# Optimization experiments

Hardware: AMD Instinct MI355X
Metric: run time of the kernel (lower is better)

Reference implementation:

```python
import jax, jax.numpy as jnp
import numpy as np

N_NODES = 50000
N_EDGES = 1600000
IN_FEAT = 256
HIDDEN = 128
N_CLASSES = 16


def gcn_conv(x, edge_index, W, b, n_nodes):
    """PyG GCNConv: x' = D^{-1/2} (A+I) D^{-1/2} (x @ W) + b."""
    h = x @ W  # project first (PyG order), messages are in out_dim
    src, dst = edge_index[0], edge_index[1]
    loops = jnp.arange(n_nodes, dtype=src.dtype)
    src = jnp.concatenate([src, loops])
    dst = jnp.concatenate([dst, loops])
    # degree of A+I (count incoming edges incl. self loop)
    deg = jax.ops.segment_sum(jnp.ones_like(dst, dtype=h.dtype), dst, num_segments=n_nodes)
    dis = jax.lax.rsqrt(deg)  # deg >= 1 thanks to self loops
    norm = dis[src] * dis[dst]  # [E+N]
    msgs = h[src] * norm[:, None]  # gather + scale
    out = jax.ops.segment_sum(msgs, dst, num_segments=n_nodes)  # scatter-add
    return out + b


def setup_inputs() -> dict:
    key = jax.random.key(0)
    k_x, k_e, k_w1, k_b1, k_w2, k_b2 = jax.random.split(key, 6)
    x = jax.random.normal(k_x, (N_NODES, IN_FEAT), dtype=jnp.float32)
    edge_index = jax.random.randint(k_e, (2, N_EDGES), 0, N_NODES, dtype=jnp.int64)
    s1 = 1.0 / np.sqrt(IN_FEAT)
    s2 = 1.0 / np.sqrt(HIDDEN)
    W1 = jax.random.uniform(k_w1, (IN_FEAT, HIDDEN), jnp.float32, -s1, s1)
    b1 = jax.random.uniform(k_b1, (HIDDEN,), jnp.float32, -s1, s1)
    W2 = jax.random.uniform(k_w2, (HIDDEN, N_CLASSES), jnp.float32, -s2, s2)
    b2 = jax.random.uniform(k_b2, (N_CLASSES,), jnp.float32, -s2, s2)
    return {"x": x, "edge_index": edge_index, "W1": W1, "b1": b1, "W2": W2, "b2": b2}


def reference(x, edge_index, W1, b1, W2, b2):
    n = x.shape[0]
    h = gcn_conv(x, edge_index, W1, b1, n)
    h = jax.nn.relu(h)
    logits = gcn_conv(h, edge_index, W2, b2, n)
    return logits, jax.nn.softmax(logits, axis=1)
```

## Files before the change

kernel.cpp:

```cpp
#include <hip/hip_runtime.h>
#include <hip/hip_bf16.h>
#include <math.h>

#define N_NODES 50000
#define N_EDGES 1600000
#define IN_FEAT 256
#define HIDDEN 128
#define N_CLASSES 16

#define ECHUNK 8192
#define NCHK 196
#define NBKT 196

typedef __attribute__((ext_vector_type(8))) short short8;
typedef __attribute__((ext_vector_type(4))) float floatx4;

__device__ __forceinline__ unsigned short f2bf(float f) {
    unsigned u = __float_as_uint(f);
    return (unsigned short)((u + 0x7fffu + ((u >> 16) & 1u)) >> 16);
}

__device__ __forceinline__ unsigned pk2bf(float a, float b) {
    __hip_bfloat162 h = __float22bfloat162_rn(make_float2(a, b));
    union { __hip_bfloat162 h; unsigned u; } cv;
    cv.h = h;
    return cv.u;
}


__global__ __launch_bounds__(256) void edge_hist(const int* __restrict__ dst,
                                                 int* __restrict__ hist,
                                                 const float* __restrict__ W1,
                                                 unsigned short* __restrict__ w1t) {
    __shared__ int h[256];
    int t = threadIdx.x;
    h[t] = 0;
    if (blockIdx.x < HIDDEN)
        w1t[blockIdx.x * IN_FEAT + t] = f2bf(W1[t * HIDDEN + blockIdx.x]);
    __syncthreads();
    int base = blockIdx.x * ECHUNK;
    int end = min(base + ECHUNK, N_EDGES);
    for (int i = base + t; i < end; i += 256)
        atomicAdd(&h[dst[i] >> 8], 1);
    __syncthreads();
    hist[blockIdx.x * 256 + t] = h[t];
}

__global__ __launch_bounds__(256) void scan_hist(int* __restrict__ hist,
                                                 int* __restrict__ bucket_base) {
    __shared__ int tot[256];
    int b = threadIdx.x;
    int sum = 0;
    for (int c = 0; c < NCHK; ++c) sum += hist[c * 256 + b];
    int v = sum;
    tot[b] = sum;
    __syncthreads();
    for (int off = 1; off < 256; off <<= 1) {
        int x = (b >= off) ? tot[b - off] : 0;
        __syncthreads();
        tot[b] += x;
        __syncthreads();
    }
    int excl = tot[b] - v;
    bucket_base[b] = excl;
    int run = excl;
    for (int c = 0; c < NCHK; ++c) {
        int h = hist[c * 256 + b];
        hist[c * 256 + b] = run;
        run += h;
    }
}

__global__ __launch_bounds__(256) void scatter_edges(const int* __restrict__ src,
                                                     const int* __restrict__ dst,
                                                     const int* __restrict__ hist,
                                                     unsigned int* __restrict__ sorted) {
    __shared__ int cur[256];
    int t = threadIdx.x;
    cur[t] = hist[blockIdx.x * 256 + t];
    __syncthreads();
    int base = blockIdx.x * ECHUNK;
    int end = min(base + ECHUNK, N_EDGES);
    for (int i = base + t; i < end; i += 256) {
        int d = dst[i];
        int s = src[i];
        int pos = atomicAdd(&cur[d >> 8], 1);
        sorted[pos] = ((unsigned)d << 16) | (unsigned)s;
    }
}

__global__ __launch_bounds__(256) void build_csr(const unsigned int* __restrict__ sorted,
                                                 const int* __restrict__ bucket_base,
                                                 int* __restrict__ row_start,
                                                 float* __restrict__ dis,
                                                 unsigned short* __restrict__ csr_src) {
    __shared__ int cnt[256];
    __shared__ int roff[256];
    int t = threadIdx.x;
    int bkt = blockIdx.x;
    int ebase = bucket_base[bkt];
    int eend = (bkt == NBKT - 1) ? N_EDGES : bucket_base[bkt + 1];
    cnt[t] = 0;
    __syncthreads();
    for (int i = ebase + t; i < eend; i += 256)
        atomicAdd(&cnt[(sorted[i] >> 16) & 255], 1);
    __syncthreads();
    int v = cnt[t];
    roff[t] = v;
    __syncthreads();
    for (int off = 1; off < 256; off <<= 1) {
        int x = (t >= off) ? roff[t - off] : 0;
        __syncthreads();
        roff[t] += x;
        __syncthreads();
    }
    int excl = roff[t] - v;
    int node = bkt * 256 + t;
    if (node < N_NODES) {
        row_start[node] = ebase + excl;
        dis[node] = 1.0f / sqrtf((float)(v + 1));
        if (node == N_NODES - 1) row_start[N_NODES] = N_EDGES;
    }
    __syncthreads();
    cnt[t] = ebase + excl;
    __syncthreads();
    for (int i = ebase + t; i < eend; i += 256) {
        unsigned e = sorted[i];
        int pos = atomicAdd(&cnt[(e >> 16) & 255], 1);
        csr_src[pos] = (unsigned short)(e & 0xffffu);
    }
}

__global__ __launch_bounds__(256) void gemm1_mfma(const float* __restrict__ x,
                                                  const unsigned short* __restrict__ w1t,
                                                  const float* __restrict__ dis,
                                                  unsigned int* __restrict__ g1) {
    int tid = threadIdx.x;
    int w = tid >> 6;
    int lane = tid & 63;
    int quad = lane >> 4;
    int c = lane & 15;
    int row_base = blockIdx.x * 64 + (w >> 1) * 32;
    int col_base = (w & 1) * 64;

    floatx4 acc[2][4] = {};

    const float* xp[2];
#pragma unroll
    for (int rt = 0; rt < 2; ++rt) {
        int r = min(row_base + rt * 16 + c, N_NODES - 1);
        xp[rt] = x + (size_t)r * IN_FEAT + quad * 8;
    }
    const unsigned short* bp[4];
#pragma unroll
    for (int nt = 0; nt < 4; ++nt)
        bp[nt] = w1t + (size_t)(col_base + nt * 16 + c) * IN_FEAT + quad * 8;

#pragma unroll
    for (int k0 = 0; k0 < IN_FEAT; k0 += 32) {
        short8 a[2], b[4];
#pragma unroll
        for (int rt = 0; rt < 2; ++rt) {
            float4 f0 = *(const float4*)(xp[rt] + k0);
            float4 f1 = *(const float4*)(xp[rt] + k0 + 4);
            union { short8 s; unsigned u[4]; } au;
            au.u[0] = pk2bf(f0.x, f0.y);
            au.u[1] = pk2bf(f0.z, f0.w);
            au.u[2] = pk2bf(f1.x, f1.y);
            au.u[3] = pk2bf(f1.z, f1.w);
            a[rt] = au.s;
        }
#pragma unroll
        for (int nt = 0; nt < 4; ++nt)
            b[nt] = *(const short8*)(bp[nt] + k0);
#pragma unroll
        for (int rt = 0; rt < 2; ++rt)
#pragma unroll
            for (int nt = 0; nt < 4; ++nt)
                acc[rt][nt] = __builtin_amdgcn_mfma_f32_16x16x32_bf16(a[rt], b[nt], acc[rt][nt], 0, 0, 0);
    }

    bool evenlane = (lane & 1) == 0;
#pragma unroll
    for (int rt = 0; rt < 2; ++rt) {
#pragma unroll
        for (int reg = 0; reg < 4; ++reg) {
            int row = row_base + rt * 16 + quad * 4 + reg;
            float dv = dis[min(row, N_NODES - 1)];
#pragma unroll
            for (int nt = 0; nt < 4; ++nt) {
                float v = acc[rt][nt][reg] * dv;
                float vo = __shfl_xor(v, 1);
                if (evenlane && row < N_NODES) {
                    unsigned pkd = (unsigned)f2bf(v) | ((unsigned)f2bf(vo) << 16);
                    g1[(size_t)row * 64 + (col_base >> 1) + nt * 8 + (c >> 1)] = pkd;
                }
            }
        }
    }
}

__global__ __launch_bounds__(256) void agg1_gemm2(const unsigned int* __restrict__ g1,
                                                  const int* __restrict__ row_start,
                                                  const unsigned short* __restrict__ csr_src,
                                                  const float* __restrict__ dis,
                                                  const float* __restrict__ b1,
                                                  const float* __restrict__ W2,
                                                  float* __restrict__ g2) {
    __shared__ float w2s[HIDDEN * N_CLASSES];
    __shared__ float rs[4][HIDDEN];
    int tid = threadIdx.x;
    for (int i = tid; i < HIDDEN * N_CLASSES; i += 256) w2s[i] = W2[i];
    __syncthreads();

    int wave = tid >> 6;
    int lane = tid & 63;
    int node = blockIdx.x * 4 + wave;

    unsigned su = g1[(size_t)node * 64 + lane];
    float a0x = __uint_as_float(su << 16), a0y = __uint_as_float(su & 0xffff0000u);
    float a1x = 0.f, a1y = 0.f, a2x = 0.f, a2y = 0.f, a3x = 0.f, a3y = 0.f;
    float a4x = 0.f, a4y = 0.f, a5x = 0.f, a5y = 0.f, a6x = 0.f, a6y = 0.f, a7x = 0.f, a7y = 0.f;

    int e0 = row_start[node], e1 = row_start[node + 1];
    int e = e0;
    for (; e + 8 <= e1; e += 8) {
        int s0 = csr_src[e + 0], s1 = csr_src[e + 1], s2 = csr_src[e + 2], s3 = csr_src[e + 3];
        int s4 = csr_src[e + 4], s5 = csr_src[e + 5], s6 = csr_src[e + 6], s7 = csr_src[e + 7];
        unsigned u0 = g1[(size_t)s0 * 64 + lane];
        unsigned u1 = g1[(size_t)s1 * 64 + lane];
        unsigned u2 = g1[(size_t)s2 * 64 + lane];
        unsigned u3 = g1[(size_t)s3 * 64 + lane];
        unsigned u4 = g1[(size_t)s4 * 64 + lane];
        unsigned u5 = g1[(size_t)s5 * 64 + lane];
        unsigned u6 = g1[(size_t)s6 * 64 + lane];
        unsigned u7 = g1[(size_t)s7 * 64 + lane];
        a0x += __uint_as_float(u0 << 16); a0y += __uint_as_float(u0 & 0xffff0000u);
        a1x += __uint_as_float(u1 << 16); a1y += __uint_as_float(u1 & 0xffff0000u);
        a2x += __uint_as_float(u2 << 16); a2y += __uint_as_float(u2 & 0xffff0000u);
        a3x += __uint_as_float(u3 << 16); a3y += __uint_as_float(u3 & 0xffff0000u);
        a4x += __uint_as_float(u4 << 16); a4y += __uint_as_float(u4 & 0xffff0000u);
        a5x += __uint_as_float(u5 << 16); a5y += __uint_as_float(u5 & 0xffff0000u);
        a6x += __uint_as_float(u6 << 16); a6y += __uint_as_float(u6 & 0xffff0000u);
        a7x += __uint_as_float(u7 << 16); a7y += __uint_as_float(u7 & 0xffff0000u);
    }
    for (; e < e1; ++e) {
        int s = csr_src[e];
        unsigned u = g1[(size_t)s * 64 + lane];
        a0x += __uint_as_float(u << 16); a0y += __uint_as_float(u & 0xffff0000u);
    }
    float sx = ((a0x + a1x) + (a2x + a3x)) + ((a4x + a5x) + (a6x + a7x));
    float sy = ((a0y + a1y) + (a2y + a3y)) + ((a4y + a5y) + (a6y + a7y));

    float dv = dis[node];
    float2 bb = ((const float2*)b1)[lane];
    float rx = fmaxf(fmaf(dv, sx, bb.x), 0.f);
    float ry = fmaxf(fmaf(dv, sy, bb.y), 0.f);

    *(float2*)&rs[wave][lane * 2] = make_float2(rx, ry);

    int grp = lane >> 4;
    int c = lane & 15;
    int f0 = grp * 32;
    float p = 0.f;
#pragma unroll
    for (int k = 0; k < 32; ++k)
        p = fmaf(rs[wave][f0 + k], w2s[(f0 + k) * N_CLASSES + c], p);
    p += __shfl_xor(p, 16);
    p += __shfl_xor(p, 32);
    if (lane < 16) g2[(size_t)node * N_CLASSES + lane] = dv * p;
}

__global__ __launch_bounds__(256) void agg2_softmax(const float* __restrict__ g2,
                                                    const int* __restrict__ row_start,
                                                    const unsigned short* __restrict__ csr_src,
                                                    const float* __restrict__ dis,
                                                    const float* __restrict__ b2,
                                                    float* __restrict__ out) {
    int tid = threadIdx.x;
    int node = blockIdx.x * 16 + (tid >> 4);
    int c = tid & 15;
    float acc0 = g2[(size_t)node * N_CLASSES + c];
    float acc1 = 0.f, acc2 = 0.f, acc3 = 0.f;
    float acc4 = 0.f, acc5 = 0.f, acc6 = 0.f, acc7 = 0.f;
    int e0 = row_start[node], e1 = row_start[node + 1];
    int e = e0;
    for (; e + 8 <= e1; e += 8) {
        int s0 = csr_src[e + 0], s1 = csr_src[e + 1], s2 = csr_src[e + 2], s3 = csr_src[e + 3];
        int s4 = csr_src[e + 4], s5 = csr_src[e + 5], s6 = csr_src[e + 6], s7 = csr_src[e + 7];
        acc0 += g2[(size_t)s0 * N_CLASSES + c];
        acc1 += g2[(size_t)s1 * N_CLASSES + c];
        acc2 += g2[(size_t)s2 * N_CLASSES + c];
        acc3 += g2[(size_t)s3 * N_CLASSES + c];
        acc4 += g2[(size_t)s4 * N_CLASSES + c];
        acc5 += g2[(size_t)s5 * N_CLASSES + c];
        acc6 += g2[(size_t)s6 * N_CLASSES + c];
        acc7 += g2[(size_t)s7 * N_CLASSES + c];
    }
    for (; e < e1; ++e) {
        int s = csr_src[e];
        acc0 += g2[(size_t)s * N_CLASSES + c];
    }
    acc0 = ((acc0 + acc1) + (acc2 + acc3)) + ((acc4 + acc5) + (acc6 + acc7));
    float logit = fmaf(dis[node], acc0, b2[c]);
    out[(size_t)node * N_CLASSES + c] = logit;
    float m = logit;
    for (int off = 8; off; off >>= 1) m = fmaxf(m, __shfl_xor(m, off));
    float ex = expf(logit - m);
    float s = ex;
    for (int off = 8; off; off >>= 1) s += __shfl_xor(s, off);
    out[(size_t)N_NODES * N_CLASSES + (size_t)node * N_CLASSES + c] = ex / s;
}


extern "C" void kernel_launch(void* const* d_in, const int* in_sizes, int n_in,
                              void* d_out, int out_size, void* d_ws, size_t ws_size,
                              hipStream_t stream) {
    const float* x  = (const float*)d_in[0];
    const int*   ei = (const int*)d_in[1];
    const float* W1 = (const float*)d_in[2];
    const float* b1 = (const float*)d_in[3];
    const float* W2 = (const float*)d_in[4];
    const float* b2 = (const float*)d_in[5];
    float* out = (float*)d_out;

    char* ws = (char*)d_ws;
    size_t off = 0;
    auto alloc = [&](size_t bytes) -> char* {
        char* p = ws + off;
        off = (off + bytes + 511) & ~(size_t)511;
        return p;
    };
    int*   hist        = (int*)alloc((size_t)NCHK * 256 * 4);
    int*   bucket_base = (int*)alloc(256 * 4);
    float* dis         = (float*)alloc(N_NODES * 4);
    int*   row_start   = (int*)alloc((N_NODES + 1) * 4);
    unsigned short* w1t = (unsigned short*)alloc((size_t)HIDDEN * IN_FEAT * 2);
    unsigned short* csr_src = (unsigned short*)alloc((size_t)N_EDGES * 2);
    unsigned int* g1   = (unsigned int*)alloc((size_t)N_NODES * 64 * 4);
    float* g2          = (float*)alloc((size_t)N_NODES * N_CLASSES * 4);
    unsigned int* sorted = (unsigned int*)g1;
    (void)ws_size; (void)in_sizes; (void)n_in; (void)out_size;

    const int* src = ei;
    const int* dst = ei + N_EDGES;

    edge_hist<<<NCHK, 256, 0, stream>>>(dst, hist, W1, w1t);
    scan_hist<<<1, 256, 0, stream>>>(hist, bucket_base);
    scatter_edges<<<NCHK, 256, 0, stream>>>(src, dst, hist, sorted);
    build_csr<<<NBKT, 256, 0, stream>>>(sorted, bucket_base, row_start, dis, csr_src);

    gemm1_mfma<<<(N_NODES + 63) / 64, 256, 0, stream>>>(x, w1t, dis, g1);
    agg1_gemm2<<<N_NODES / 4, 256, 0, stream>>>(g1, row_start, csr_src, dis, b1, W2, g2);
    agg2_softmax<<<N_NODES / 16, 256, 0, stream>>>(g2, row_start, csr_src, dis, b2, out);
}
```

Before: 259.6 us.

## Replace histogram-scan edge sort with fixed-capacity atomic buckets; prefetch gemm1 operands

```diff
diff --git a/kernel.cpp b/kernel.cpp
--- a/kernel.cpp
+++ b/kernel.cpp
@@ -11,6 +11,7 @@
 #define ECHUNK 8192
 #define NCHK 196
 #define NBKT 196
+#define BCAP 10240
 
 typedef __attribute__((ext_vector_type(8))) short short8;
 typedef __attribute__((ext_vector_type(4))) float floatx4;
@@ -27,79 +28,48 @@
     return cv.u;
 }
 
-
-__global__ __launch_bounds__(256) void edge_hist(const int* __restrict__ dst,
-                                                 int* __restrict__ hist,
-                                                 const float* __restrict__ W1,
-                                                 unsigned short* __restrict__ w1t) {
-    __shared__ int h[256];
+__global__ __launch_bounds__(256) void scatter_edges2(const int* __restrict__ src,
+                                                      const int* __restrict__ dst,
+                                                      int* __restrict__ cursor,
+                                                      unsigned int* __restrict__ sorted,
+                                                      const float* __restrict__ W1,
+                                                      unsigned short* __restrict__ w1t) {
+    __shared__ int hloc[256];
     int t = threadIdx.x;
-    h[t] = 0;
+    hloc[t] = 0;
     if (blockIdx.x < HIDDEN)
         w1t[blockIdx.x * IN_FEAT + t] = f2bf(W1[t * HIDDEN + blockIdx.x]);
     __syncthreads();
     int base = blockIdx.x * ECHUNK;
     int end = min(base + ECHUNK, N_EDGES);
     for (int i = base + t; i < end; i += 256)
-        atomicAdd(&h[dst[i] >> 8], 1);
-    __syncthreads();
-    hist[blockIdx.x * 256 + t] = h[t];
-}
-
-__global__ __launch_bounds__(256) void scan_hist(int* __restrict__ hist,
-                                                 int* __restrict__ bucket_base) {
-    __shared__ int tot[256];
-    int b = threadIdx.x;
-    int sum = 0;
-    for (int c = 0; c < NCHK; ++c) sum += hist[c * 256 + b];
-    int v = sum;
-    tot[b] = sum;
-    __syncthreads();
-    for (int off = 1; off < 256; off <<= 1) {
-        int x = (b >= off) ? tot[b - off] : 0;
-        __syncthreads();
-        tot[b] += x;
-        __syncthreads();
-    }
-    int excl = tot[b] - v;
-    bucket_base[b] = excl;
-    int run = excl;
-    for (int c = 0; c < NCHK; ++c) {
-        int h = hist[c * 256 + b];
-        hist[c * 256 + b] = run;
-        run += h;
-    }
-}
-
-__global__ __launch_bounds__(256) void scatter_edges(const int* __restrict__ src,
-                                                     const int* __restrict__ dst,
-                                                     const int* __restrict__ hist,
-                                                     unsigned int* __restrict__ sorted) {
-    __shared__ int cur[256];
-    int t = threadIdx.x;
-    cur[t] = hist[blockIdx.x * 256 + t];
-    __syncthreads();
-    int base = blockIdx.x * ECHUNK;
-    int end = min(base + ECHUNK, N_EDGES);
+        atomicAdd(&hloc[dst[i] >> 8], 1);
+    __syncthreads();
+    int cnt = hloc[t];
+    int lbase = t * BCAP + atomicAdd(&cursor[t], cnt);
+    __syncthreads();
+    hloc[t] = lbase;
+    __syncthreads();
     for (int i = base + t; i < end; i += 256) {
         int d = dst[i];
         int s = src[i];
-        int pos = atomicAdd(&cur[d >> 8], 1);
+        int pos = atomicAdd(&hloc[d >> 8], 1);
         sorted[pos] = ((unsigned)d << 16) | (unsigned)s;
     }
 }
 
-__global__ __launch_bounds__(256) void build_csr(const unsigned int* __restrict__ sorted,
-                                                 const int* __restrict__ bucket_base,
-                                                 int* __restrict__ row_start,
-                                                 float* __restrict__ dis,
-                                                 unsigned short* __restrict__ csr_src) {
+__global__ __launch_bounds__(256) void build_csr2(const unsigned int* __restrict__ sorted,
+                                                  const int* __restrict__ cursor,
+                                                  int* __restrict__ rs,
+                                                  int* __restrict__ re,
+                                                  float* __restrict__ dis,
+                                                  unsigned short* __restrict__ csr_src) {
     __shared__ int cnt[256];
     __shared__ int roff[256];
     int t = threadIdx.x;
     int bkt = blockIdx.x;
-    int ebase = bucket_base[bkt];
-    int eend = (bkt == NBKT - 1) ? N_EDGES : bucket_base[bkt + 1];
+    int ebase = bkt * BCAP;
+    int eend = ebase + cursor[bkt];
     cnt[t] = 0;
     __syncthreads();
     for (int i = ebase + t; i < eend; i += 256)
@@ -117,9 +87,9 @@
     int excl = roff[t] - v;
     int node = bkt * 256 + t;
     if (node < N_NODES) {
-        row_start[node] = ebase + excl;
+        rs[node] = ebase + excl;
+        re[node] = ebase + excl + v;
         dis[node] = 1.0f / sqrtf((float)(v + 1));
-        if (node == N_NODES - 1) row_start[N_NODES] = N_EDGES;
     }
     __syncthreads();
     cnt[t] = ebase + excl;
@@ -156,28 +126,53 @@
     for (int nt = 0; nt < 4; ++nt)
         bp[nt] = w1t + (size_t)(col_base + nt * 16 + c) * IN_FEAT + quad * 8;
 
-#pragma unroll
-    for (int k0 = 0; k0 < IN_FEAT; k0 += 32) {
-        short8 a[2], b[4];
+    float4 fa[2][2];
+    short8 bcur[4];
+#pragma unroll
+    for (int rt = 0; rt < 2; ++rt) {
+        fa[rt][0] = *(const float4*)(xp[rt] + 0);
+        fa[rt][1] = *(const float4*)(xp[rt] + 4);
+    }
+#pragma unroll
+    for (int nt = 0; nt < 4; ++nt)
+        bcur[nt] = *(const short8*)(bp[nt] + 0);
+
+#pragma unroll
+    for (int kk = 0; kk < 8; ++kk) {
+        float4 fn[2][2];
+        short8 bn[4];
+        if (kk < 7) {
+            int k0n = (kk + 1) * 32;
+#pragma unroll
+            for (int rt = 0; rt < 2; ++rt) {
+                fn[rt][0] = *(const float4*)(xp[rt] + k0n);
+                fn[rt][1] = *(const float4*)(xp[rt] + k0n + 4);
+            }
+#pragma unroll
+            for (int nt = 0; nt < 4; ++nt)
+                bn[nt] = *(const short8*)(bp[nt] + k0n);
+        }
+        short8 a[2];
 #pragma unroll
         for (int rt = 0; rt < 2; ++rt) {
-            float4 f0 = *(const float4*)(xp[rt] + k0);
-            float4 f1 = *(const float4*)(xp[rt] + k0 + 4);
             union { short8 s; unsigned u[4]; } au;
-            au.u[0] = pk2bf(f0.x, f0.y);
-            au.u[1] = pk2bf(f0.z, f0.w);
-            au.u[2] = pk2bf(f1.x, f1.y);
-            au.u[3] = pk2bf(f1.z, f1.w);
+            au.u[0] = pk2bf(fa[rt][0].x, fa[rt][0].y);
+            au.u[1] = pk2bf(fa[rt][0].z, fa[rt][0].w);
+            au.u[2] = pk2bf(fa[rt][1].x, fa[rt][1].y);
+            au.u[3] = pk2bf(fa[rt][1].z, fa[rt][1].w);
             a[rt] = au.s;
         }
 #pragma unroll
-        for (int nt = 0; nt < 4; ++nt)
-            b[nt] = *(const short8*)(bp[nt] + k0);
-#pragma unroll
         for (int rt = 0; rt < 2; ++rt)
 #pragma unroll
             for (int nt = 0; nt < 4; ++nt)
-                acc[rt][nt] = __builtin_amdgcn_mfma_f32_16x16x32_bf16(a[rt], b[nt], acc[rt][nt], 0, 0, 0);
+                acc[rt][nt] = __builtin_amdgcn_mfma_f32_16x16x32_bf16(a[rt], bcur[nt], acc[rt][nt], 0, 0, 0);
+        if (kk < 7) {
+#pragma unroll
+            for (int rt = 0; rt < 2; ++rt) { fa[rt][0] = fn[rt][0]; fa[rt][1] = fn[rt][1]; }
+#pragma unroll
+            for (int nt = 0; nt < 4; ++nt) bcur[nt] = bn[nt];
+        }
     }
 
     bool evenlane = (lane & 1) == 0;
@@ -201,14 +196,15 @@
 }
 
 __global__ __launch_bounds__(256) void agg1_gemm2(const unsigned int* __restrict__ g1,
-                                                  const int* __restrict__ row_start,
+                                                  const int* __restrict__ rs,
+                                                  const int* __restrict__ re,
                                                   const unsigned short* __restrict__ csr_src,
                                                   const float* __restrict__ dis,
                                                   const float* __restrict__ b1,
                                                   const float* __restrict__ W2,
                                                   float* __restrict__ g2) {
     __shared__ float w2s[HIDDEN * N_CLASSES];
-    __shared__ float rs[4][HIDDEN];
+    __shared__ float rsh[4][HIDDEN];
     int tid = threadIdx.x;
     for (int i = tid; i < HIDDEN * N_CLASSES; i += 256) w2s[i] = W2[i];
     __syncthreads();
@@ -222,7 +218,7 @@
     float a1x = 0.f, a1y = 0.f, a2x = 0.f, a2y = 0.f, a3x = 0.f, a3y = 0.f;
     float a4x = 0.f, a4y = 0.f, a5x = 0.f, a5y = 0.f, a6x = 0.f, a6y = 0.f, a7x = 0.f, a7y = 0.f;
 
-    int e0 = row_start[node], e1 = row_start[node + 1];
+    int e0 = rs[node], e1 = re[node];
     int e = e0;
     for (; e + 8 <= e1; e += 8) {
         int s0 = csr_src[e + 0], s1 = csr_src[e + 1], s2 = csr_src[e + 2], s3 = csr_src[e + 3];
@@ -257,7 +253,7 @@
     float rx = fmaxf(fmaf(dv, sx, bb.x), 0.f);
     float ry = fmaxf(fmaf(dv, sy, bb.y), 0.f);
 
-    *(float2*)&rs[wave][lane * 2] = make_float2(rx, ry);
+    *(float2*)&rsh[wave][lane * 2] = make_float2(rx, ry);
 
     int grp = lane >> 4;
     int c = lane & 15;
@@ -265,14 +261,15 @@
     float p = 0.f;
 #pragma unroll
     for (int k = 0; k < 32; ++k)
-        p = fmaf(rs[wave][f0 + k], w2s[(f0 + k) * N_CLASSES + c], p);
+        p = fmaf(rsh[wave][f0 + k], w2s[(f0 + k) * N_CLASSES + c], p);
     p += __shfl_xor(p, 16);
     p += __shfl_xor(p, 32);
     if (lane < 16) g2[(size_t)node * N_CLASSES + lane] = dv * p;
 }
 
 __global__ __launch_bounds__(256) void agg2_softmax(const float* __restrict__ g2,
-                                                    const int* __restrict__ row_start,
+                                                    const int* __restrict__ rs,
+                                                    const int* __restrict__ re,
                                                     const unsigned short* __restrict__ csr_src,
                                                     const float* __restrict__ dis,
                                                     const float* __restrict__ b2,
@@ -283,7 +280,7 @@
     float acc0 = g2[(size_t)node * N_CLASSES + c];
     float acc1 = 0.f, acc2 = 0.f, acc3 = 0.f;
     float acc4 = 0.f, acc5 = 0.f, acc6 = 0.f, acc7 = 0.f;
-    int e0 = row_start[node], e1 = row_start[node + 1];
+    int e0 = rs[node], e1 = re[node];
     int e = e0;
     for (; e + 8 <= e1; e += 8) {
         int s0 = csr_src[e + 0], s1 = csr_src[e + 1], s2 = csr_src[e + 2], s3 = csr_src[e + 3];
@@ -331,26 +328,25 @@
         off = (off + bytes + 511) & ~(size_t)511;
         return p;
     };
-    int*   hist        = (int*)alloc((size_t)NCHK * 256 * 4);
-    int*   bucket_base = (int*)alloc(256 * 4);
-    float* dis         = (float*)alloc(N_NODES * 4);
-    int*   row_start   = (int*)alloc((N_NODES + 1) * 4);
+    int*   cursor   = (int*)alloc(256 * 4);
+    float* dis      = (float*)alloc(N_NODES * 4);
+    int*   rs       = (int*)alloc(N_NODES * 4);
+    int*   re       = (int*)alloc(N_NODES * 4);
     unsigned short* w1t = (unsigned short*)alloc((size_t)HIDDEN * IN_FEAT * 2);
-    unsigned short* csr_src = (unsigned short*)alloc((size_t)N_EDGES * 2);
-    unsigned int* g1   = (unsigned int*)alloc((size_t)N_NODES * 64 * 4);
-    float* g2          = (float*)alloc((size_t)N_NODES * N_CLASSES * 4);
+    unsigned short* csr_src = (unsigned short*)alloc((size_t)NBKT * BCAP * 2);
+    unsigned int* g1 = (unsigned int*)alloc((size_t)N_NODES * 64 * 4);
+    float* g2       = (float*)alloc((size_t)N_NODES * N_CLASSES * 4);
     unsigned int* sorted = (unsigned int*)g1;
     (void)ws_size; (void)in_sizes; (void)n_in; (void)out_size;
 
     const int* src = ei;
     const int* dst = ei + N_EDGES;
 
-    edge_hist<<<NCHK, 256, 0, stream>>>(dst, hist, W1, w1t);
-    scan_hist<<<1, 256, 0, stream>>>(hist, bucket_base);
-    scatter_edges<<<NCHK, 256, 0, stream>>>(src, dst, hist, sorted);
-    build_csr<<<NBKT, 256, 0, stream>>>(sorted, bucket_base, row_start, dis, csr_src);
+    hipMemsetAsync(cursor, 0, 256 * 4, stream);
+    scatter_edges2<<<NCHK, 256, 0, stream>>>(src, dst, cursor, sorted, W1, w1t);
+    build_csr2<<<NBKT, 256, 0, stream>>>(sorted, cursor, rs, re, dis, csr_src);
 
     gemm1_mfma<<<(N_NODES + 63) / 64, 256, 0, stream>>>(x, w1t, dis, g1);
-    agg1_gemm2<<<N_NODES / 4, 256, 0, stream>>>(g1, row_start, csr_src, dis, b1, W2, g2);
-    agg2_softmax<<<N_NODES / 16, 256, 0, stream>>>(g2, row_start, csr_src, dis, b2, out);
-}
+    agg1_gemm2<<<N_NODES / 4, 256, 0, stream>>>(g1, rs, re, csr_src, dis, b1, W2, g2);
+    agg2_softmax<<<N_NODES / 16, 256, 0, stream>>>(g2, rs, re, csr_src, dis, b2, out);
+}
```

Result: faster. 249.3 us (-4.0%).
